# Kernel tuning notes

Measured on AMD Instinct MI355X. Metric: run time of the kernel, lower is better.

The kernel has to match this reference:

```python
import jax, jax.numpy as jnp
import numpy as np

B, S, D = 2, 2048, 1024
H, E = 16, 64          # n_heads, head_dim
DFF = 4096             # intermediate
R_ATTN, R_OUT, R_FF = 32, 512, 512
LN_EPS = 1e-5
SCALE = 1.0 / np.sqrt(E)


def setup_inputs() -> dict:
    key = jax.random.key(0)
    ks = jax.random.split(key, 24)
    s = 0.02
    inp = {
        "hidden_states": jax.random.normal(ks[0], (B, S, D), jnp.float32),
        "ln1_w": jnp.ones((D,), jnp.float32),
        "ln1_b": jnp.zeros((D,), jnp.float32),
        "q_U": jax.random.normal(ks[1], (H, E, R_ATTN), jnp.float32) * s,
        "q_V": jax.random.normal(ks[2], (H, R_ATTN, D), jnp.float32) * s,
        "q_bias": jax.random.normal(ks[3], (H, E), jnp.float32) * s,
        "k_U": jax.random.normal(ks[4], (H, E, R_ATTN), jnp.float32) * s,
        "k_V": jax.random.normal(ks[5], (H, R_ATTN, D), jnp.float32) * s,
        "k_bias": jax.random.normal(ks[6], (H, E), jnp.float32) * s,
        "v_U": jax.random.normal(ks[7], (H, E, R_ATTN), jnp.float32) * s,
        "v_V": jax.random.normal(ks[8], (H, R_ATTN, D), jnp.float32) * s,
        "v_bias": jax.random.normal(ks[9], (H, E), jnp.float32) * s,
        "out_U": jax.random.normal(ks[10], (D, R_OUT), jnp.float32) * s,
        "out_V": jax.random.normal(ks[11], (R_OUT, D), jnp.float32) * s,
        "out_bias": jnp.zeros((D,), jnp.float32),
        "ln2_w": jnp.ones((D,), jnp.float32),
        "ln2_b": jnp.zeros((D,), jnp.float32),
        "fc1_U": jax.random.normal(ks[12], (DFF, R_FF), jnp.float32) * s,
        "fc1_V": jax.random.normal(ks[13], (R_FF, D), jnp.float32) * s,
        "fc1_bias": jnp.zeros((DFF,), jnp.float32),
        "fc2_U": jax.random.normal(ks[14], (D, R_FF), jnp.float32) * s,
        "fc2_V": jax.random.normal(ks[15], (R_FF, DFF), jnp.float32) * s,
        "fc2_bias": jnp.zeros((D,), jnp.float32),
    }
    return inp


def _layernorm(x, w, b):
    mu = jnp.mean(x, axis=-1, keepdims=True)
    var = jnp.mean(jnp.square(x - mu), axis=-1, keepdims=True)
    return (x - mu) * jax.lax.rsqrt(var + LN_EPS) * w + b


def _per_head_svd(x, U, V, bias):
    # x: [b,s,d]; V: [h,r,d]; U: [h,e,r]; bias: [h,e] -> [b,h,s,e]
    t = jnp.einsum("bsd,hrd->bhsr", x, V)
    return jnp.einsum("bhsr,her->bhse", t, U) + bias[None, :, None, :]


def reference(hidden_states, ln1_w, ln1_b, q_U, q_V, q_bias, k_U, k_V, k_bias,
              v_U, v_V, v_bias, out_U, out_V, out_bias, ln2_w, ln2_b,
              fc1_U, fc1_V, fc1_bias, fc2_U, fc2_V, fc2_bias):
    b, s, d = hidden_states.shape
    normed = _layernorm(hidden_states, ln1_w, ln1_b)

    q = _per_head_svd(normed, q_U, q_V, q_bias)  # [b,h,s,e]
    k = _per_head_svd(normed, k_U, k_V, k_bias)
    v = _per_head_svd(normed, v_U, v_V, v_bias)

    scores = jnp.einsum("bhqe,bhke->bhqk", q, k) * SCALE
    causal = jnp.tril(jnp.ones((s, s), dtype=bool))
    scores = jnp.where(causal, scores, -jnp.inf)
    probs = jax.nn.softmax(scores, axis=-1)
    attn = jnp.einsum("bhqk,bhke->bhqe", probs, v)
    attn = attn.transpose(0, 2, 1, 3).reshape(b, s, d)  # [b,s,d]

    attn = jnp.einsum("bsr,dr->bsd", jnp.einsum("bsd,rd->bsr", attn, out_V), out_U) + out_bias
    hidden_states = hidden_states + attn

    normed = _layernorm(hidden_states, ln2_w, ln2_b)
    ff = jnp.einsum("bsr,fr->bsf", jnp.einsum("bsd,rd->bsr", normed, fc1_V), fc1_U) + fc1_bias
    ff = jax.nn.gelu(ff, approximate=False)  # exact erf gelu as in torch F.gelu
    ff = jnp.einsum("bsr,dr->bsd", jnp.einsum("bsf,rf->bsr", ff, fc2_V), fc2_U) + fc2_bias
    hidden_states = hidden_states + ff
    return (hidden_states,)
```

## Files before the change

kernel.cpp:

```cpp
#include <hip/hip_runtime.h>
#include <hip/hip_bf16.h>
#include <math.h>

#define Bc 2
#define Sc 2048
#define Dc 1024
#define Hc 16
#define Ec 64
#define DFFc 4096
#define SCALEc 0.125f
#define SCLOG2E 0.18033688f
#define LN_EPSc 1e-5f
#define BH_STRIDE 131072

typedef short bf16x8 __attribute__((ext_vector_type(8)));
typedef unsigned short u16x4 __attribute__((ext_vector_type(4)));
typedef unsigned short u16x8 __attribute__((ext_vector_type(8)));
typedef float f32x4 __attribute__((ext_vector_type(4)));
typedef float f32x16 __attribute__((ext_vector_type(16)));
typedef unsigned int u32x4 __attribute__((ext_vector_type(4)));
#define MFMA16(a, b, c) __builtin_amdgcn_mfma_f32_16x16x32_bf16(a, b, c, 0, 0, 0)
#define MFMA32(a, b, c) __builtin_amdgcn_mfma_f32_32x32x16_bf16(a, b, c, 0, 0, 0)
#define GLDS16(g, l)                                                            \
  __builtin_amdgcn_global_load_lds((const __attribute__((address_space(1))) void*)(g), \
                                   (__attribute__((address_space(3))) void*)(l), 16, 0, 0)

static __device__ __forceinline__ unsigned short f2bf(float x) {
  unsigned u = __float_as_uint(x);
  unsigned r = (u + 0x7FFFu + ((u >> 16) & 1u)) >> 16;
  return (unsigned short)r;
}
static __device__ __forceinline__ unsigned cvtpk(float lo, float hi) {
  unsigned r;
  asm("v_cvt_pk_bf16_f32 %0, %1, %2" : "=v"(r) : "v"(lo), "v"(hi));
  return r;
}

__global__ __launch_bounds__(256) void prep(
    const float* __restrict__ s0, const float* __restrict__ s1, const float* __restrict__ s2,
    const float* __restrict__ s3, const float* __restrict__ s4, const float* __restrict__ s5,
    const float* __restrict__ s6, const float* __restrict__ s7, const float* __restrict__ s8,
    unsigned short* __restrict__ wsu,
    const float* __restrict__ x, const float* __restrict__ lw, const float* __restrict__ lb,
    unsigned short* __restrict__ nout) {
  __shared__ float sm[8];
  int tid = threadIdx.x;
  if (blockIdx.x < 7680) {
    int i = (blockIdx.x * 256 + tid) * 4;
    const float* s;
    int off;
    if (i < 3145728) {
      int seg = i >> 19;
      off = i & 524287;
      s = (seg == 0) ? s0 : (seg == 1) ? s1 : (seg == 2) ? s2
          : (seg == 3) ? s3 : (seg == 4) ? s4 : s5;
    } else if (i < 5242880) { s = s6; off = i - 3145728; }
    else if (i < 7340032)   { s = s7; off = i - 5242880; }
    else if (i < 7864320)   { s = s8; off = i - 7340032; }
    else return;
    float4 v = *(const float4*)(s + off);
    u16x4 o = {f2bf(v.x), f2bf(v.y), f2bf(v.z), f2bf(v.w)};
    *(u16x4*)(wsu + i) = o;
    return;
  }
  int row = blockIdx.x - 7680;
  const float* xr = x + (size_t)row * Dc;
  float v[4];
  float sum = 0.f;
#pragma unroll
  for (int i = 0; i < 4; ++i) { v[i] = xr[tid + i * 256]; sum += v[i]; }
#pragma unroll
  for (int off = 32; off > 0; off >>= 1) sum += __shfl_down(sum, off, 64);
  if ((tid & 63) == 0) sm[tid >> 6] = sum;
  __syncthreads();
  float mean = (sm[0] + sm[1] + sm[2] + sm[3]) * (1.f / Dc);
  float var = 0.f;
#pragma unroll
  for (int i = 0; i < 4; ++i) { float d0 = v[i] - mean; var += d0 * d0; }
#pragma unroll
  for (int off = 32; off > 0; off >>= 1) var += __shfl_down(var, off, 64);
  if ((tid & 63) == 0) sm[4 + (tid >> 6)] = var;
  __syncthreads();
  float rstd = rsqrtf((sm[4] + sm[5] + sm[6] + sm[7]) * (1.f / Dc) + LN_EPSc);
  unsigned short* orow = nout + (size_t)row * Dc;
#pragma unroll
  for (int i = 0; i < 4; ++i) {
    int c = tid + i * 256;
    orow[c] = f2bf((v[i] - mean) * rstd * lw[c] + lb[c]);
  }
}

__global__ __launch_bounds__(256) void ln_bf16(const float* __restrict__ x,
                                               const float* __restrict__ w,
                                               const float* __restrict__ b,
                                               unsigned short* __restrict__ out) {
  __shared__ float sm[8];
  int row = blockIdx.x;
  int tid = threadIdx.x;
  const float* xr = x + (size_t)row * Dc;
  float v[4];
  float sum = 0.f;
#pragma unroll
  for (int i = 0; i < 4; ++i) { v[i] = xr[tid + i * 256]; sum += v[i]; }
#pragma unroll
  for (int off = 32; off > 0; off >>= 1) sum += __shfl_down(sum, off, 64);
  if ((tid & 63) == 0) sm[tid >> 6] = sum;
  __syncthreads();
  float mean = (sm[0] + sm[1] + sm[2] + sm[3]) * (1.f / Dc);
  float var = 0.f;
#pragma unroll
  for (int i = 0; i < 4; ++i) { float d0 = v[i] - mean; var += d0 * d0; }
#pragma unroll
  for (int off = 32; off > 0; off >>= 1) var += __shfl_down(var, off, 64);
  if ((tid & 63) == 0) sm[4 + (tid >> 6)] = var;
  __syncthreads();
  float rstd = rsqrtf((sm[4] + sm[5] + sm[6] + sm[7]) * (1.f / Dc) + LN_EPSc);
  unsigned short* orow = out + (size_t)row * Dc;
#pragma unroll
  for (int i = 0; i < 4; ++i) {
    int c = tid + i * 256;
    orow[c] = f2bf((v[i] - mean) * rstd * w[c] + b[c]);
  }
}

template <int BM, int BN>
__global__ __launch_bounds__(256) void gemm_bf16(const unsigned short* __restrict__ A,
                                                 const unsigned short* __restrict__ W,
                                                 float* __restrict__ Cf,
                                                 unsigned short* __restrict__ Cb,
                                                 const float* __restrict__ bias,
                                                 const float* __restrict__ res,
                                                 int M, int N, int K, int gelu, int nbm) {
  constexpr int BK = 64;
  constexpr int MT = BM / 32;
  constexpr int NT = BN / 32;
  __shared__ unsigned short As[2][BM * BK];
  __shared__ unsigned short Bs[2][BN * BK];
  int tid = threadIdx.x;
  int lane = tid & 63;
  int wid = tid >> 6;
  int cl = lane & 15, grp = lane >> 4;
  int wr = wid >> 1, wc = wid & 1;
  int bm = blockIdx.x % nbm;
  int bn = blockIdx.x / nbm;
  const unsigned short* Ab = A + (size_t)(bm * BM) * K;
  const unsigned short* Wb = W + (size_t)(bn * BN) * K;
  f32x4 acc[MT][NT];
  f32x4 z4 = {0.f, 0.f, 0.f, 0.f};
#pragma unroll
  for (int i = 0; i < MT; ++i)
#pragma unroll
    for (int j = 0; j < NT; ++j) acc[i][j] = z4;
  int r0 = tid >> 3;
  int c0 = (tid & 7) * 8;

#define STAGE(buf, k0)                                                         \
  {                                                                            \
    _Pragma("unroll") for (int l = 0; l < BM / 32; ++l) {                      \
      int row = r0 + l * 32;                                                   \
      int sc = c0 ^ ((row & 7) * 8);                                           \
      GLDS16(Ab + (size_t)row * K + (k0) + sc, &As[buf][(tid + l * 256) * 8]); \
    }                                                                          \
    _Pragma("unroll") for (int l = 0; l < BN / 32; ++l) {                      \
      int row = r0 + l * 32;                                                   \
      int sc = c0 ^ ((row & 7) * 8);                                           \
      GLDS16(Wb + (size_t)row * K + (k0) + sc, &Bs[buf][(tid + l * 256) * 8]); \
    }                                                                          \
  }

  int nt = K / BK;
  STAGE(0, 0)
  __syncthreads();
  for (int t = 0; t < nt; ++t) {
    int cur = t & 1;
    if (t + 1 < nt) STAGE(cur ^ 1, (t + 1) * BK)
#pragma unroll
    for (int kk = 0; kk < 2; ++kk) {
      bf16x8 af[MT], bfr[NT];
#pragma unroll
      for (int i = 0; i < MT; ++i) {
        int row = wr * (BM / 2) + i * 16 + cl;
        af[i] = *(const bf16x8*)&As[cur][row * BK + ((kk * 32 + grp * 8) ^ ((row & 7) * 8))];
      }
#pragma unroll
      for (int j = 0; j < NT; ++j) {
        int row = wc * (BN / 2) + j * 16 + cl;
        bfr[j] = *(const bf16x8*)&Bs[cur][row * BK + ((kk * 32 + grp * 8) ^ ((row & 7) * 8))];
      }
#pragma unroll
      for (int i = 0; i < MT; ++i)
#pragma unroll
        for (int j = 0; j < NT; ++j) acc[i][j] = MFMA16(af[i], bfr[j], acc[i][j]);
    }
    __syncthreads();
  }
#undef STAGE

#pragma unroll
  for (int i = 0; i < MT; ++i) {
    int row = bm * BM + wr * (BM / 2) + i * 16 + grp * 4;
#pragma unroll
    for (int j = 0; j < NT; ++j) {
      int col = bn * BN + wc * (BN / 2) + j * 16 + cl;
      float bv = bias ? bias[col] : 0.f;
#pragma unroll
      for (int r = 0; r < 4; ++r) {
        float v = acc[i][j][r] + bv;
        if (gelu) v = 0.5f * v * (1.f + erff(v * 0.70710678118f));
        if (res) v += res[(size_t)(row + r) * N + col];
        if (Cb) Cb[(size_t)(row + r) * N + col] = f2bf(v);
        else Cf[(size_t)(row + r) * N + col] = v;
      }
    }
  }
}

template <int BM, int BN>
__global__ __launch_bounds__(256) void gemm_splitk2(const unsigned short* __restrict__ A,
                                                    const unsigned short* __restrict__ W,
                                                    float* __restrict__ P0,
                                                    float* __restrict__ P1,
                                                    int M, int N, int K, int nbm) {
  constexpr int BK = 64;
  constexpr int MT = BM / 32;
  constexpr int NT = BN / 32;
  __shared__ unsigned short As[2][BM * BK];
  __shared__ unsigned short Bs[2][BN * BK];
  int tid = threadIdx.x;
  int lane = tid & 63;
  int wid = tid >> 6;
  int cl = lane & 15, grp = lane >> 4;
  int wr = wid >> 1, wc = wid & 1;
  int per = nbm * (N / BN);
  int slice = blockIdx.x / per;
  int inner = blockIdx.x % per;
  int bm = inner % nbm;
  int bn = inner / nbm;
  int Ks = K / 2;
  const unsigned short* Ab = A + (size_t)(bm * BM) * K + (size_t)slice * Ks;
  const unsigned short* Wb = W + (size_t)(bn * BN) * K + (size_t)slice * Ks;
  float* P = slice ? P1 : P0;
  f32x4 acc[MT][NT];
  f32x4 z4 = {0.f, 0.f, 0.f, 0.f};
#pragma unroll
  for (int i = 0; i < MT; ++i)
#pragma unroll
    for (int j = 0; j < NT; ++j) acc[i][j] = z4;
  int r0 = tid >> 3;
  int c0 = (tid & 7) * 8;

#define STAGE(buf, k0)                                                         \
  {                                                                            \
    _Pragma("unroll") for (int l = 0; l < BM / 32; ++l) {                      \
      int row = r0 + l * 32;                                                   \
      int sc = c0 ^ ((row & 7) * 8);                                           \
      GLDS16(Ab + (size_t)row * K + (k0) + sc, &As[buf][(tid + l * 256) * 8]); \
    }                                                                          \
    _Pragma("unroll") for (int l = 0; l < BN / 32; ++l) {                      \
      int row = r0 + l * 32;                                                   \
      int sc = c0 ^ ((row & 7) * 8);                                           \
      GLDS16(Wb + (size_t)row * K + (k0) + sc, &Bs[buf][(tid + l * 256) * 8]); \
    }                                                                          \
  }

  int nt = Ks / BK;
  STAGE(0, 0)
  __syncthreads();
  for (int t = 0; t < nt; ++t) {
    int cur = t & 1;
    if (t + 1 < nt) STAGE(cur ^ 1, (t + 1) * BK)
#pragma unroll
    for (int kk = 0; kk < 2; ++kk) {
      bf16x8 af[MT], bfr[NT];
#pragma unroll
      for (int i = 0; i < MT; ++i) {
        int row = wr * (BM / 2) + i * 16 + cl;
        af[i] = *(const bf16x8*)&As[cur][row * BK + ((kk * 32 + grp * 8) ^ ((row & 7) * 8))];
      }
#pragma unroll
      for (int j = 0; j < NT; ++j) {
        int row = wc * (BN / 2) + j * 16 + cl;
        bfr[j] = *(const bf16x8*)&Bs[cur][row * BK + ((kk * 32 + grp * 8) ^ ((row & 7) * 8))];
      }
#pragma unroll
      for (int i = 0; i < MT; ++i)
#pragma unroll
        for (int j = 0; j < NT; ++j) acc[i][j] = MFMA16(af[i], bfr[j], acc[i][j]);
    }
    __syncthreads();
  }
#undef STAGE

#pragma unroll
  for (int i = 0; i < MT; ++i) {
    int row = bm * BM + wr * (BM / 2) + i * 16 + grp * 4;
#pragma unroll
    for (int j = 0; j < NT; ++j) {
      int col = bn * BN + wc * (BN / 2) + j * 16 + cl;
#pragma unroll
      for (int r = 0; r < 4; ++r)
        P[(size_t)(row + r) * N + col] = acc[i][j][r];
    }
  }
}

__global__ __launch_bounds__(256) void reduce2(const float* __restrict__ P0,
                                               const float* __restrict__ P1,
                                               unsigned short* __restrict__ out, int n) {
  int i = (blockIdx.x * 256 + threadIdx.x) * 4;
  if (i >= n) return;
  float4 a = *(const float4*)(P0 + i);
  float4 b = *(const float4*)(P1 + i);
  u16x4 o = {f2bf(a.x + b.x), f2bf(a.y + b.y), f2bf(a.z + b.z), f2bf(a.w + b.w)};
  *(u16x4*)(out + i) = o;
}

__global__ __launch_bounds__(256) void expand_all(const float* __restrict__ t,
                                                  const float* __restrict__ qU,
                                                  const float* __restrict__ kU,
                                                  const float* __restrict__ vU,
                                                  const float* __restrict__ qB,
                                                  const float* __restrict__ kB,
                                                  const float* __restrict__ vB,
                                                  unsigned short* __restrict__ qO,
                                                  unsigned short* __restrict__ kO,
                                                  unsigned short* __restrict__ vO) {
  __shared__ float Us[64][33];
  __shared__ float Ts[32][33];
  int blk = blockIdx.x;
  int kind = blk >> 11;
  int inner = blk & 2047;
  int sb = inner & 63;
  int h = (inner >> 6) & 15;
  int b = inner >> 10;
  int bh = b * Hc + h;
  int tid = threadIdx.x;
  const float* U = (kind == 0) ? qU : (kind == 1) ? kU : vU;
  const float* bias = (kind == 0) ? qB : (kind == 1) ? kB : vB;
  int toff = kind * 512;
  for (int i = tid; i < 64 * 32; i += 256) Us[i >> 5][i & 31] = U[h * 2048 + i];
  for (int i = tid; i < 32 * 32; i += 256) {
    int sr = i >> 5, r = i & 31;
    Ts[sr][r] = t[(size_t)(b * Sc + sb * 32 + sr) * 1536 + toff + h * 32 + r];
  }
  __syncthreads();
  if (kind < 2) {
    unsigned short* out = (kind == 0) ? qO : kO;
    float prescale = (kind == 0) ? SCLOG2E : 1.0f;
    int s = tid >> 3;
    int ec = tid & 7;
    float acc[8];
#pragma unroll
    for (int j = 0; j < 8; ++j) acc[j] = bias[h * 64 + ec * 8 + j];
    for (int r = 0; r < 32; ++r) {
      float tv = Ts[s][r];
#pragma unroll
      for (int j = 0; j < 8; ++j) acc[j] += tv * Us[ec * 8 + j][r];
    }
    u16x8 v8;
#pragma unroll
    for (int j = 0; j < 8; ++j) v8[j] = f2bf(acc[j] * prescale);
    int es = ec >> 1, hi = ec & 1;
    int lane = s + hi * 32;
    *(u16x8*)(out + (size_t)bh * BH_STRIDE + (size_t)(((sb * 4 + es) * 64 + lane)) * 8) = v8;
  } else {
    int e = tid & 63;
    int sg = tid >> 6;
    float bv = bias[h * 64 + e];
    u16x8 v8;
#pragma unroll
    for (int si = 0; si < 8; ++si) {
      int sr = sg * 8 + si;
      float acc = bv;
#pragma unroll
      for (int r = 0; r < 32; ++r) acc += Ts[sr][r] * Us[e][r];
      v8[si] = f2bf(acc);
    }
    int eo = e >> 5, ll = e & 31;
    int h2 = sg >> 1, hi = sg & 1;
    int ix = eo * 2 + h2;
    int lane = ll + hi * 32;
    *(u16x8*)(vO + (size_t)bh * BH_STRIDE + (size_t)(((sb * 4 + ix) * 64 + lane)) * 8) = v8;
  }
}

__global__ __launch_bounds__(256) void attn_mfma(const unsigned short* __restrict__ qf_,
                                                 const unsigned short* __restrict__ kf_,
                                                 const unsigned short* __restrict__ vf_,
                                                 unsigned short* __restrict__ out) {
  __shared__ float MS[2][33][64];
  int tid = threadIdx.x;
  int wid = tid >> 6;
  int lane = tid & 63;
  int ll = lane & 31;
  int hi = lane >> 5;
  int bid = blockIdx.x;
  int xcd = bid & 7;
  int idx = bid >> 3;
  int qt = 63 - (idx >> 2);
  int bh = xcd + 8 * (idx & 3);
  int b = bh >> 4, h = bh & 15;
  const unsigned short* qb = qf_ + (size_t)bh * BH_STRIDE;
  const unsigned short* kb = kf_ + (size_t)bh * BH_STRIDE;
  const unsigned short* vb = vf_ + (size_t)bh * BH_STRIDE;
  int q0 = qt * 32;
  int nt = qt + 1;
  int full = nt - 1;
  int fs = wid * full / 4;
  int fe = (wid + 1) * full / 4;

  bf16x8 qf[4];
#pragma unroll
  for (int es = 0; es < 4; ++es)
    qf[es] = *(const bf16x8*)(qb + (size_t)((qt * 4 + es) * 64 + lane) * 8);

  f32x16 accO[2] = {};
  f32x16 lacc = {};

  int t = fs;
  for (; t + 1 < fe; t += 2) {
    bf16x8 ka[4], kb2[4];
#pragma unroll
    for (int es = 0; es < 4; ++es) {
      ka[es] = *(const bf16x8*)(kb + (size_t)((t * 4 + es) * 64 + lane) * 8);
      kb2[es] = *(const bf16x8*)(kb + (size_t)(((t + 1) * 4 + es) * 64 + lane) * 8);
    }
    f32x16 cA = {}, cB = {};
    __builtin_amdgcn_s_setprio(1);
    cA = MFMA32(ka[0], qf[0], cA);
    cA = MFMA32(ka[1], qf[1], cA);
    cA = MFMA32(ka[2], qf[2], cA);
    cA = MFMA32(ka[3], qf[3], cA);
    cB = MFMA32(kb2[0], qf[0], cB);
    cB = MFMA32(kb2[1], qf[1], cB);
    cB = MFMA32(kb2[2], qf[2], cB);
    cB = MFMA32(kb2[3], qf[3], cB);
    __builtin_amdgcn_s_setprio(0);
    float pA[16], pB[16];
#pragma unroll
    for (int r = 0; r < 16; ++r) { pA[r] = exp2f(cA[r]); pB[r] = exp2f(cB[r]); }
#pragma unroll
    for (int r = 0; r < 16; ++r) lacc[r] += pA[r] + pB[r];
    bf16x8 va[4], vb2[4];
#pragma unroll
    for (int ix = 0; ix < 4; ++ix) {
      va[ix] = *(const bf16x8*)(vb + (size_t)((t * 4 + ix) * 64 + lane) * 8);
      vb2[ix] = *(const bf16x8*)(vb + (size_t)(((t + 1) * 4 + ix) * 64 + lane) * 8);
    }
    unsigned wA0 = cvtpk(pA[0], pA[1]), wA1 = cvtpk(pA[2], pA[3]);
    unsigned wA2 = cvtpk(pA[4], pA[5]), wA3 = cvtpk(pA[6], pA[7]);
    unsigned wA4 = cvtpk(pA[8], pA[9]), wA5 = cvtpk(pA[10], pA[11]);
    unsigned wA6 = cvtpk(pA[12], pA[13]), wA7 = cvtpk(pA[14], pA[15]);
    unsigned wB0 = cvtpk(pB[0], pB[1]), wB1 = cvtpk(pB[2], pB[3]);
    unsigned wB2 = cvtpk(pB[4], pB[5]), wB3 = cvtpk(pB[6], pB[7]);
    unsigned wB4 = cvtpk(pB[8], pB[9]), wB5 = cvtpk(pB[10], pB[11]);
    unsigned wB6 = cvtpk(pB[12], pB[13]), wB7 = cvtpk(pB[14], pB[15]);
    asm("v_permlane32_swap_b32 %0, %1" : "+v"(wA0), "+v"(wA2));
    asm("v_permlane32_swap_b32 %0, %1" : "+v"(wA1), "+v"(wA3));
    asm("v_permlane32_swap_b32 %0, %1" : "+v"(wA4), "+v"(wA6));
    asm("v_permlane32_swap_b32 %0, %1" : "+v"(wA5), "+v"(wA7));
    asm("v_permlane32_swap_b32 %0, %1" : "+v"(wB0), "+v"(wB2));
    asm("v_permlane32_swap_b32 %0, %1" : "+v"(wB1), "+v"(wB3));
    asm("v_permlane32_swap_b32 %0, %1" : "+v"(wB4), "+v"(wB6));
    asm("v_permlane32_swap_b32 %0, %1" : "+v"(wB5), "+v"(wB7));
    u32x4 pA0v = {wA0, wA1, wA2, wA3}, pA1v = {wA4, wA5, wA6, wA7};
    u32x4 pB0v = {wB0, wB1, wB2, wB3}, pB1v = {wB4, wB5, wB6, wB7};
    bf16x8 bA0 = __builtin_bit_cast(bf16x8, pA0v), bA1 = __builtin_bit_cast(bf16x8, pA1v);
    bf16x8 bB0 = __builtin_bit_cast(bf16x8, pB0v), bB1 = __builtin_bit_cast(bf16x8, pB1v);
    __builtin_amdgcn_s_setprio(1);
    accO[0] = MFMA32(va[0], bA0, accO[0]);
    accO[0] = MFMA32(va[1], bA1, accO[0]);
    accO[0] = MFMA32(vb2[0], bB0, accO[0]);
    accO[0] = MFMA32(vb2[1], bB1, accO[0]);
    accO[1] = MFMA32(va[2], bA0, accO[1]);
    accO[1] = MFMA32(va[3], bA1, accO[1]);
    accO[1] = MFMA32(vb2[2], bB0, accO[1]);
    accO[1] = MFMA32(vb2[3], bB1, accO[1]);
    __builtin_amdgcn_s_setprio(0);
  }

#define ATT_ONE(T, MASKED)                                                          \
  {                                                                                 \
    bf16x8 kf1[4];                                                                  \
    _Pragma("unroll") for (int es = 0; es < 4; ++es)                                \
      kf1[es] = *(const bf16x8*)(kb + (size_t)(((T) * 4 + es) * 64 + lane) * 8);    \
    f32x16 c = {};                                                                  \
    __builtin_amdgcn_s_setprio(1);                                                  \
    c = MFMA32(kf1[0], qf[0], c);                                                   \
    c = MFMA32(kf1[1], qf[1], c);                                                   \
    c = MFMA32(kf1[2], qf[2], c);                                                   \
    c = MFMA32(kf1[3], qf[3], c);                                                   \
    __builtin_amdgcn_s_setprio(0);                                                  \
    float p1[16];                                                                   \
    _Pragma("unroll") for (int r = 0; r < 16; ++r) {                                \
      if (MASKED) {                                                                 \
        int keyloc = (r & 3) + 8 * (r >> 2) + 4 * hi;                               \
        p1[r] = (keyloc > ll) ? 0.f : exp2f(c[r]);                                  \
      } else p1[r] = exp2f(c[r]);                                                   \
    }                                                                               \
    _Pragma("unroll") for (int r = 0; r < 16; ++r) lacc[r] += p1[r];                \
    bf16x8 vf1[4];                                                                  \
    _Pragma("unroll") for (int ix = 0; ix < 4; ++ix)                                \
      vf1[ix] = *(const bf16x8*)(vb + (size_t)(((T) * 4 + ix) * 64 + lane) * 8);    \
    unsigned w0 = cvtpk(p1[0], p1[1]), w1 = cvtpk(p1[2], p1[3]);                    \
    unsigned w2 = cvtpk(p1[4], p1[5]), w3 = cvtpk(p1[6], p1[7]);                    \
    unsigned w4 = cvtpk(p1[8], p1[9]), w5 = cvtpk(p1[10], p1[11]);                  \
    unsigned w6 = cvtpk(p1[12], p1[13]), w7 = cvtpk(p1[14], p1[15]);                \
    asm("v_permlane32_swap_b32 %0, %1" : "+v"(w0), "+v"(w2));                       \
    asm("v_permlane32_swap_b32 %0, %1" : "+v"(w1), "+v"(w3));                       \
    asm("v_permlane32_swap_b32 %0, %1" : "+v"(w4), "+v"(w6));                       \
    asm("v_permlane32_swap_b32 %0, %1" : "+v"(w5), "+v"(w7));                       \
    u32x4 pw0 = {w0, w1, w2, w3};                                                   \
    u32x4 pw1 = {w4, w5, w6, w7};                                                   \
    bf16x8 pb0 = __builtin_bit_cast(bf16x8, pw0);                                   \
    bf16x8 pb1 = __builtin_bit_cast(bf16x8, pw1);                                   \
    __builtin_amdgcn_s_setprio(1);                                                  \
    accO[0] = MFMA32(vf1[0], pb0, accO[0]);                                         \
    accO[0] = MFMA32(vf1[1], pb1, accO[0]);                                         \
    accO[1] = MFMA32(vf1[2], pb0, accO[1]);                                         \
    accO[1] = MFMA32(vf1[3], pb1, accO[1]);                                         \
    __builtin_amdgcn_s_setprio(0);                                                  \
  }

  if (t < fe) ATT_ONE(t, false)
  if (wid == 3) ATT_ONE(full, true)
#undef ATT_ONE

  float l;
  {
    float s8[8];
#pragma unroll
    for (int r = 0; r < 8; ++r) s8[r] = lacc[r] + lacc[r + 8];
    float s4a = s8[0] + s8[4], s4b = s8[1] + s8[5], s4c = s8[2] + s8[6], s4d = s8[3] + s8[7];
    l = (s4a + s4b) + (s4c + s4d);
  }

  auto publish = [&](int slot) {
#pragma unroll
    for (int r = 0; r < 16; ++r) {
      MS[slot][r][lane] = accO[0][r];
      MS[slot][16 + r][lane] = accO[1][r];
    }
    MS[slot][32][lane] = l;
  };
  auto merge = [&](int slot) {
    l += MS[slot][32][lane];
#pragma unroll
    for (int r = 0; r < 16; ++r) {
      accO[0][r] += MS[slot][r][lane];
      accO[1][r] += MS[slot][16 + r][lane];
    }
  };
  if (wid == 1) publish(0);
  if (wid == 3) publish(1);
  __syncthreads();
  if (wid == 0) merge(0);
  if (wid == 2) merge(1);
  __syncthreads();
  if (wid == 2) publish(0);
  __syncthreads();
  if (wid == 0) {
    merge(0);
    float ltot = l + __shfl_xor(l, 32, 64);
    float inv = 1.f / ltot;
    unsigned short* orow = out + (size_t)(b * Sc + q0 + ll) * Dc + h * Ec;
#pragma unroll
    for (int eo = 0; eo < 2; ++eo)
#pragma unroll
      for (int g = 0; g < 4; ++g) {
        u16x4 o4 = {f2bf(accO[eo][4 * g + 0] * inv), f2bf(accO[eo][4 * g + 1] * inv),
                    f2bf(accO[eo][4 * g + 2] * inv), f2bf(accO[eo][4 * g + 3] * inv)};
        *(u16x4*)(orow + eo * 32 + 8 * g + 4 * hi) = o4;
      }
  }
}

extern "C" void kernel_launch(void* const* d_in, const int* in_sizes, int n_in,
                              void* d_out, int out_size, void* d_ws, size_t ws_size,
                              hipStream_t stream) {
  const float* hidden = (const float*)d_in[0];
  const float* ln1_w = (const float*)d_in[1];
  const float* ln1_b = (const float*)d_in[2];
  const float* q_U = (const float*)d_in[3];
  const float* q_V = (const float*)d_in[4];
  const float* q_bias = (const float*)d_in[5];
  const float* k_U = (const float*)d_in[6];
  const float* k_V = (const float*)d_in[7];
  const float* k_bias = (const float*)d_in[8];
  const float* v_U = (const float*)d_in[9];
  const float* v_V = (const float*)d_in[10];
  const float* v_bias = (const float*)d_in[11];
  const float* out_U = (const float*)d_in[12];
  const float* out_V = (const float*)d_in[13];
  const float* out_bias = (const float*)d_in[14];
  const float* ln2_w = (const float*)d_in[15];
  const float* ln2_b = (const float*)d_in[16];
  const float* fc1_U = (const float*)d_in[17];
  const float* fc1_V = (const float*)d_in[18];
  const float* fc1_bias = (const float*)d_in[19];
  const float* fc2_U = (const float*)d_in[20];
  const float* fc2_V = (const float*)d_in[21];
  const float* fc2_bias = (const float*)d_in[22];
  float* out = (float*)d_out;
  float* ws = (float*)d_ws;
  unsigned short* wsu = (unsigned short*)d_ws;

  unsigned short* wQKV = wsu;
  unsigned short* wOUTV = wsu + 1572864;
  unsigned short* wOUTU = wsu + 2097152;
  unsigned short* wFC1V = wsu + 2621440;
  unsigned short* wFC1U = wsu + 3145728;
  unsigned short* wFC2V = wsu + 5242880;
  unsigned short* wFC2U = wsu + 7340032;

  float* h1 = ws + 4194304;
  unsigned short* attn_out = (unsigned short*)(ws + 6291456);
  unsigned short* normed = (unsigned short*)(ws + 8388608);
  float* rb = ws + 10485760;
  unsigned short* rbB = (unsigned short*)(ws + 10485760);
  unsigned short* ff = (unsigned short*)(ws + 11534336);
  unsigned short* qbuf = (unsigned short*)(ws + 16777216);
  unsigned short* kbuf = (unsigned short*)(ws + 18874368);
  unsigned short* vtbuf = (unsigned short*)(ws + 20971520);
  float* P0f = ws + 8388608;
  float* P1f = ws + 19922944;
  unsigned short* rbG2 = (unsigned short*)(ws + 10485760);

  const int M = Bc * Sc;
  dim3 blk(256);

  prep<<<7680 + M, blk, 0, stream>>>(q_V, k_V, v_V, out_V, out_U, fc1_V, fc1_U, fc2_V, fc2_U,
                                     wsu, hidden, ln1_w, ln1_b, normed);

  gemm_bf16<64, 64><<<1536, blk, 0, stream>>>(normed, wQKV, rb, nullptr, nullptr, nullptr,
                                              M, 1536, Dc, 0, 64);
  expand_all<<<6144, blk, 0, stream>>>(rb, q_U, k_U, v_U, q_bias, k_bias, v_bias,
                                       qbuf, kbuf, vtbuf);

  attn_mfma<<<2048, blk, 0, stream>>>(qbuf, kbuf, vtbuf, attn_out);

  gemm_bf16<64, 32><<<1024, blk, 0, stream>>>(attn_out, wOUTV, nullptr, rbB, nullptr, nullptr,
                                              M, 512, Dc, 0, 64);
  gemm_bf16<64, 64><<<1024, blk, 0, stream>>>(rbB, wOUTU, h1, nullptr, out_bias, hidden,
                                              M, Dc, 512, 0, 64);

  ln_bf16<<<M, blk, 0, stream>>>(h1, ln2_w, ln2_b, normed);
  gemm_bf16<64, 32><<<1024, blk, 0, stream>>>(normed, wFC1V, nullptr, rbB, nullptr, nullptr,
                                              M, 512, Dc, 0, 64);
  gemm_bf16<128, 64><<<2048, blk, 0, stream>>>(rbB, wFC1U, nullptr, ff, fc1_bias, nullptr,
                                               M, DFFc, 512, 1, 32);
  gemm_splitk2<64, 64><<<1024, blk, 0, stream>>>(ff, wFC2V, P0f, P1f, M, 512, DFFc, 64);
  reduce2<<<2048, blk, 0, stream>>>(P0f, P1f, rbG2, M * 512);
  gemm_bf16<64, 64><<<1024, blk, 0, stream>>>(rbG2, wFC2U, out, nullptr, fc2_bias, h1,
                                              M, Dc, 512, 0, 64);
}
```

Before: 252.9 us.

## Precompute dense QKV weights from low-rank factors and use single GEMM

```diff
diff --git a/kernel.cpp b/kernel.cpp
--- a/kernel.cpp
+++ b/kernel.cpp
@@ -37,33 +37,42 @@
 }
 
 __global__ __launch_bounds__(256) void prep(
-    const float* __restrict__ s0, const float* __restrict__ s1, const float* __restrict__ s2,
     const float* __restrict__ s3, const float* __restrict__ s4, const float* __restrict__ s5,
     const float* __restrict__ s6, const float* __restrict__ s7, const float* __restrict__ s8,
     unsigned short* __restrict__ wsu,
     const float* __restrict__ x, const float* __restrict__ lw, const float* __restrict__ lb,
-    unsigned short* __restrict__ nout) {
+    unsigned short* __restrict__ nout,
+    const float* __restrict__ qB, const float* __restrict__ kB, const float* __restrict__ vB,
+    float* __restrict__ biasF) {
   __shared__ float sm[8];
   int tid = threadIdx.x;
-  if (blockIdx.x < 7680) {
+  if (blockIdx.x < 6144) {
     int i = (blockIdx.x * 256 + tid) * 4;
     const float* s;
     int off;
-    if (i < 3145728) {
+    if (i < 1572864) {
       int seg = i >> 19;
       off = i & 524287;
-      s = (seg == 0) ? s0 : (seg == 1) ? s1 : (seg == 2) ? s2
-          : (seg == 3) ? s3 : (seg == 4) ? s4 : s5;
-    } else if (i < 5242880) { s = s6; off = i - 3145728; }
-    else if (i < 7340032)   { s = s7; off = i - 5242880; }
-    else if (i < 7864320)   { s = s8; off = i - 7340032; }
-    else return;
+      s = (seg == 0) ? s3 : (seg == 1) ? s4 : s5;
+    } else if (i < 3670016) { s = s6; off = i - 1572864; }
+    else if (i < 5767168)   { s = s7; off = i - 3670016; }
+    else                    { s = s8; off = i - 5767168; }
     float4 v = *(const float4*)(s + off);
     u16x4 o = {f2bf(v.x), f2bf(v.y), f2bf(v.z), f2bf(v.w)};
-    *(u16x4*)(wsu + i) = o;
+    *(u16x4*)(wsu + 1572864 + i) = o;
     return;
   }
-  int row = blockIdx.x - 7680;
+  if (blockIdx.x >= 6144 + 4096) {
+    int k = blockIdx.x - 6144 - 4096;
+    const float* src = (k == 0) ? qB : (k == 1) ? kB : vB;
+    float sc = (k == 0) ? SCLOG2E : 1.0f;
+    int i = tid * 4;
+    float4 v = *(const float4*)(src + i);
+    float4 o = {v.x * sc, v.y * sc, v.z * sc, v.w * sc};
+    *(float4*)(biasF + k * 1024 + i) = o;
+    return;
+  }
+  int row = blockIdx.x - 6144;
   const float* xr = x + (size_t)row * Dc;
   float v[4];
   float sum = 0.f;
@@ -87,6 +96,81 @@
   for (int i = 0; i < 4; ++i) {
     int c = tid + i * 256;
     orow[c] = f2bf((v[i] - mean) * rstd * lw[c] + lb[c]);
+  }
+}
+
+__global__ __launch_bounds__(256) void makew(const float* __restrict__ qU,
+                                             const float* __restrict__ kU,
+                                             const float* __restrict__ vU,
+                                             const float* __restrict__ qV,
+                                             const float* __restrict__ kV,
+                                             const float* __restrict__ vV,
+                                             unsigned short* __restrict__ W) {
+  int bid = blockIdx.x;
+  int kind = bid >> 8;
+  int h = (bid >> 4) & 15;
+  int dblk = bid & 15;
+  const float* U = (kind == 0) ? qU : (kind == 1) ? kU : vU;
+  const float* V = (kind == 0) ? qV : (kind == 1) ? kV : vV;
+  __shared__ float Us[64][33];
+  __shared__ float Vs[32][64];
+  int tid = threadIdx.x;
+  for (int i = tid; i < 2048; i += 256) Us[i >> 5][i & 31] = U[h * 2048 + i];
+  for (int i = tid; i < 2048; i += 256) {
+    int r = i >> 6, d = i & 63;
+    Vs[r][d] = V[h * 32768 + r * 1024 + dblk * 64 + d];
+  }
+  __syncthreads();
+  int e = tid & 63;
+  int dq = tid >> 6;
+  float scale = (kind == 0) ? SCLOG2E : 1.0f;
+  float acc[16] = {};
+  for (int r = 0; r < 32; ++r) {
+    float u = Us[e][r];
+#pragma unroll
+    for (int j = 0; j < 16; ++j) acc[j] += u * Vs[r][dq * 16 + j];
+  }
+  u16x8 o0, o1;
+#pragma unroll
+  for (int j = 0; j < 8; ++j) {
+    o0[j] = f2bf(acc[j] * scale);
+    o1[j] = f2bf(acc[8 + j] * scale);
+  }
+  size_t base = ((size_t)(kind * 1024 + h * 64 + e)) * 1024 + dblk * 64 + dq * 16;
+  *(u16x8*)(W + base) = o0;
+  *(u16x8*)(W + base + 8) = o1;
+}
+
+__global__ __launch_bounds__(256) void relayout(const unsigned short* __restrict__ qkv,
+                                                unsigned short* __restrict__ qO,
+                                                unsigned short* __restrict__ kO,
+                                                unsigned short* __restrict__ vO) {
+  int blk = blockIdx.x;
+  int kind = blk >> 11;
+  int inner = blk & 2047;
+  int sb = inner & 63;
+  int h = (inner >> 6) & 15;
+  int b = inner >> 10;
+  int bh = b * Hc + h;
+  int tid = threadIdx.x;
+  if (kind < 2) {
+    unsigned short* out = (kind == 0) ? qO : kO;
+    int s = tid >> 3, ec = tid & 7;
+    u16x8 v8 = *(const u16x8*)(qkv + (size_t)(b * Sc + sb * 32 + s) * 3072 + kind * 1024 + h * 64 + ec * 8);
+    int es = ec >> 1, hi = ec & 1;
+    int lane = s + hi * 32;
+    *(u16x8*)(out + (size_t)bh * BH_STRIDE + (size_t)((sb * 4 + es) * 64 + lane) * 8) = v8;
+  } else {
+    int e = tid & 63, sg = tid >> 6;
+    u16x8 v8;
+#pragma unroll
+    for (int si = 0; si < 8; ++si)
+      v8[si] = qkv[(size_t)(b * Sc + sb * 32 + sg * 8 + si) * 3072 + 2048 + h * 64 + e];
+    int eo = e >> 5, ll = e & 31;
+    int h2 = sg >> 1, hi = sg & 1;
+    int ix = eo * 2 + h2;
+    int lane = ll + hi * 32;
+    *(u16x8*)(vO + (size_t)bh * BH_STRIDE + (size_t)((sb * 4 + ix) * 64 + lane) * 8) = v8;
   }
 }
 
@@ -313,75 +397,6 @@
   float4 b = *(const float4*)(P1 + i);
   u16x4 o = {f2bf(a.x + b.x), f2bf(a.y + b.y), f2bf(a.z + b.z), f2bf(a.w + b.w)};
   *(u16x4*)(out + i) = o;
-}
-
-__global__ __launch_bounds__(256) void expand_all(const float* __restrict__ t,
-                                                  const float* __restrict__ qU,
-                                                  const float* __restrict__ kU,
-                                                  const float* __restrict__ vU,
-                                                  const float* __restrict__ qB,
-                                                  const float* __restrict__ kB,
-                                                  const float* __restrict__ vB,
-                                                  unsigned short* __restrict__ qO,
-                                                  unsigned short* __restrict__ kO,
-                                                  unsigned short* __restrict__ vO) {
-  __shared__ float Us[64][33];
-  __shared__ float Ts[32][33];
-  int blk = blockIdx.x;
-  int kind = blk >> 11;
-  int inner = blk & 2047;
-  int sb = inner & 63;
-  int h = (inner >> 6) & 15;
-  int b = inner >> 10;
-  int bh = b * Hc + h;
-  int tid = threadIdx.x;
-  const float* U = (kind == 0) ? qU : (kind == 1) ? kU : vU;
-  const float* bias = (kind == 0) ? qB : (kind == 1) ? kB : vB;
-  int toff = kind * 512;
-  for (int i = tid; i < 64 * 32; i += 256) Us[i >> 5][i & 31] = U[h * 2048 + i];
-  for (int i = tid; i < 32 * 32; i += 256) {
-    int sr = i >> 5, r = i & 31;
-    Ts[sr][r] = t[(size_t)(b * Sc + sb * 32 + sr) * 1536 + toff + h * 32 + r];
-  }
-  __syncthreads();
-  if (kind < 2) {
-    unsigned short* out = (kind == 0) ? qO : kO;
-    float prescale = (kind == 0) ? SCLOG2E : 1.0f;
-    int s = tid >> 3;
-    int ec = tid & 7;
-    float acc[8];
-#pragma unroll
-    for (int j = 0; j < 8; ++j) acc[j] = bias[h * 64 + ec * 8 + j];
-    for (int r = 0; r < 32; ++r) {
-      float tv = Ts[s][r];
-#pragma unroll
-      for (int j = 0; j < 8; ++j) acc[j] += tv * Us[ec * 8 + j][r];
-    }
-    u16x8 v8;
-#pragma unroll
-    for (int j = 0; j < 8; ++j) v8[j] = f2bf(acc[j] * prescale);
-    int es = ec >> 1, hi = ec & 1;
-    int lane = s + hi * 32;
-    *(u16x8*)(out + (size_t)bh * BH_STRIDE + (size_t)(((sb * 4 + es) * 64 + lane)) * 8) = v8;
-  } else {
-    int e = tid & 63;
-    int sg = tid >> 6;
-    float bv = bias[h * 64 + e];
-    u16x8 v8;
-#pragma unroll
-    for (int si = 0; si < 8; ++si) {
-      int sr = sg * 8 + si;
-      float acc = bv;
-#pragma unroll
-      for (int r = 0; r < 32; ++r) acc += Ts[sr][r] * Us[e][r];
-      v8[si] = f2bf(acc);
-    }
-    int eo = e >> 5, ll = e & 31;
-    int h2 = sg >> 1, hi = sg & 1;
-    int ix = eo * 2 + h2;
-    int lane = ll + hi * 32;
-    *(u16x8*)(vO + (size_t)bh * BH_STRIDE + (size_t)(((sb * 4 + ix) * 64 + lane)) * 8) = v8;
-  }
 }
 
 __global__ __launch_bounds__(256) void attn_mfma(const unsigned short* __restrict__ qf_,
@@ -605,7 +620,6 @@
   float* ws = (float*)d_ws;
   unsigned short* wsu = (unsigned short*)d_ws;
 
-  unsigned short* wQKV = wsu;
   unsigned short* wOUTV = wsu + 1572864;
   unsigned short* wOUTU = wsu + 2097152;
   unsigned short* wFC1V = wsu + 2621440;
@@ -614,10 +628,12 @@
   unsigned short* wFC2U = wsu + 7340032;
 
   float* h1 = ws + 4194304;
+  unsigned short* Wqkv = (unsigned short*)(ws + 4194304);
+  float* qkv_biasF = ws + 6000000;
   unsigned short* attn_out = (unsigned short*)(ws + 6291456);
   unsigned short* normed = (unsigned short*)(ws + 8388608);
-  float* rb = ws + 10485760;
   unsigned short* rbB = (unsigned short*)(ws + 10485760);
+  unsigned short* qkv_out = (unsigned short*)(ws + 10485760);
   unsigned short* ff = (unsigned short*)(ws + 11534336);
   unsigned short* qbuf = (unsigned short*)(ws + 16777216);
   unsigned short* kbuf = (unsigned short*)(ws + 18874368);
@@ -629,13 +645,14 @@
   const int M = Bc * Sc;
   dim3 blk(256);
 
-  prep<<<7680 + M, blk, 0, stream>>>(q_V, k_V, v_V, out_V, out_U, fc1_V, fc1_U, fc2_V, fc2_U,
-                                     wsu, hidden, ln1_w, ln1_b, normed);
-
-  gemm_bf16<64, 64><<<1536, blk, 0, stream>>>(normed, wQKV, rb, nullptr, nullptr, nullptr,
-                                              M, 1536, Dc, 0, 64);
-  expand_all<<<6144, blk, 0, stream>>>(rb, q_U, k_U, v_U, q_bias, k_bias, v_bias,
-                                       qbuf, kbuf, vtbuf);
+  makew<<<768, blk, 0, stream>>>(q_U, k_U, v_U, q_V, k_V, v_V, Wqkv);
+  prep<<<6144 + M + 3, blk, 0, stream>>>(out_V, out_U, fc1_V, fc1_U, fc2_V, fc2_U,
+                                         wsu, hidden, ln1_w, ln1_b, normed,
+                                         q_bias, k_bias, v_bias, qkv_biasF);
+
+  gemm_bf16<64, 64><<<3072, blk, 0, stream>>>(normed, Wqkv, nullptr, qkv_out, qkv_biasF,
+                                              nullptr, M, 3072, Dc, 0, 64);
+  relayout<<<6144, blk, 0, stream>>>(qkv_out, qbuf, kbuf, vtbuf);
 
   attn_mfma<<<2048, blk, 0, stream>>>(qbuf, kbuf, vtbuf, attn_out);
 
```

New measurement: 241.8 us. 4.4% less time.
